# Optimization experiments

Measured on AMD Instinct MI355X. Metric: run time of the kernel, lower is better.

Reference implementation:

```python
import jax, jax.numpy as jnp
import numpy as np
import itertools

# ---- static configuration (matches init_kwargs) ----
LS = [0, 1, 2, 3]            # spherical harmonic degrees, parity (-1)^l
MUL = 128                    # channel multiplicity of hklm / output
N_EDGES = 16384
DIMS = [2 * l + 1 for l in LS]
Y_DIM = sum(DIMS)                        # 16
H_DIM = sum(d * MUL for d in DIMS)       # 2048
Y_OFF = np.cumsum([0] + DIMS).tolist()
H_OFF = np.cumsum([0] + [d * MUL for d in DIMS]).tolist()

# ---- real-basis O(3) Clebsch-Gordan coefficients (numpy, setup-time) ----
def _su2_generators(l):
    m = np.arange(-l, l + 1)
    Lz = np.diag(m).astype(np.complex128)
    vals = np.sqrt(l * (l + 1) - m[:-1] * (m[:-1] + 1))
    Lp = np.zeros((2 * l + 1, 2 * l + 1), np.complex128)
    Lp[np.arange(1, 2 * l + 1), np.arange(2 * l)] = vals
    Lm = Lp.T.copy()
    return (Lp + Lm) / 2.0, (Lp - Lm) / 2.0j, Lz

def _c2r(l):
    # unitary change of basis: complex SH -> real SH
    d = 2 * l + 1
    U = np.zeros((d, d), np.complex128)
    U[l, l] = 1.0
    s2 = 1.0 / np.sqrt(2.0)
    for m in range(1, l + 1):
        U[l + m, l + m] = (-1) ** m * s2
        U[l + m, l - m] = s2
        U[l - m, l + m] = -1j * (-1) ** m * s2
        U[l - m, l - m] = 1j * s2
    return U

def _real_generators(l):
    U = _c2r(l)
    return [np.real(-1j * (U @ L @ U.conj().T)) for L in _su2_generators(l)]

def _cg(l1, l2, l3):
    # invariant tensor = null space of the summed infinitesimal rotation action
    G1, G2, G3 = _real_generators(l1), _real_generators(l2), _real_generators(l3)
    d1, d2, d3 = 2 * l1 + 1, 2 * l2 + 1, 2 * l3 + 1
    I1, I2, I3 = np.eye(d1), np.eye(d2), np.eye(d3)
    rows = []
    for k in range(3):
        rows.append(np.kron(np.kron(G1[k], I2), I3)
                    + np.kron(np.kron(I1, G2[k]), I3)
                    + np.kron(np.kron(I1, I2), G3[k]))
    K = np.concatenate(rows, axis=0)
    _, s, Vt = np.linalg.svd(K)
    c = Vt[-1].reshape(d1, d2, d3)
    c = c / np.linalg.norm(c)
    c = c * np.sign(c.reshape(-1)[np.argmax(np.abs(c))])  # deterministic sign
    return c

PATHS = []
_CG_LIST = []
for (i1, l1), (i2, l2), (i3, l3) in itertools.product(enumerate(LS), enumerate(LS), enumerate(LS)):
    # triangle inequality + O3 parity selection rule ((-1)^l parities)
    if abs(l1 - l2) <= l3 <= l1 + l2 and (l1 + l2 + l3) % 2 == 0:
        PATHS.append((i1, i2, i3))
        _CG_LIST.append(_cg(l1, l2, l3))
N_PATHS = len(PATHS)                    # 23
W_DIM = N_PATHS * MUL                   # 2944
CG_OFF = np.cumsum([0] + [c.size for c in _CG_LIST]).tolist()
CGC_NP = np.concatenate([c.reshape(-1) for c in _CG_LIST]).astype(np.float32)


def setup_inputs() -> dict:
    key = jax.random.key(0)
    k1, k2, k3 = jax.random.split(key, 3)
    return {
        "Ylm": jax.random.normal(k1, (N_EDGES, Y_DIM), jnp.float32),
        "hklm": jax.random.normal(k2, (N_EDGES, H_DIM), jnp.float32),
        "weight": jax.random.normal(k3, (N_EDGES, W_DIM), jnp.float32),
        "CGC": jnp.asarray(CGC_NP),   # registered buffer in the torch module
    }


def reference(Ylm, hklm, weight, CGC):
    # segmented tensor product 'abcu,a,bu,cu' with per-path weight fused in:
    # out[n, c, u] += sum_{a,b} CG_p[a,b,c] * w_p[n,u] * Y[n,a] * h[n,b,u]
    N = Ylm.shape[0]
    out = jnp.zeros((N, H_DIM), Ylm.dtype)
    for p, (i1, i2, i3) in enumerate(PATHS):
        d1, d2, d3 = DIMS[i1], DIMS[i2], DIMS[i3]
        cg = CGC[CG_OFF[p]:CG_OFF[p + 1]].reshape(d1, d2, d3)
        y = Ylm[:, Y_OFF[i1]:Y_OFF[i1] + d1]
        h = hklm[:, H_OFF[i2]:H_OFF[i2] + d2 * MUL].reshape(N, d2, MUL)
        w = weight[:, p * MUL:(p + 1) * MUL]
        z = jnp.einsum('abc,na,nbu->ncu', cg, y, h) * w[:, None, :]
        out = out.at[:, H_OFF[i3]:H_OFF[i3] + d3 * MUL].add(z.reshape(N, d3 * MUL))
    return out
```

## Files before the change

### kernel.cpp

```cpp
#include <hip/hip_runtime.h>


#define BS 256
#define GSZ 32
#define EPB 8
#define YD 16
#define HD 2048
#define WD 2944
#define NP 23
#define NROW 99

typedef float f4 __attribute__((ext_vector_type(4)));

#define FOR_PATHS(X) \
  X(0, 0,0,0,    0,  0) \
  X(1, 0,1,1,    1,  1) \
  X(2, 0,2,2,   10,  4) \
  X(3, 0,3,3,   35,  9) \
  X(4, 1,0,1,   84, 16) \
  X(5, 1,1,0,   93, 19) \
  X(6, 1,1,2,  102, 20) \
  X(7, 1,2,1,  147, 25) \
  X(8, 1,2,3,  192, 28) \
  X(9, 1,3,2,  297, 35) \
  X(10,2,0,2,  402, 40) \
  X(11,2,1,1,  427, 45) \
  X(12,2,1,3,  472, 48) \
  X(13,2,2,0,  577, 55) \
  X(14,2,2,2,  602, 56) \
  X(15,2,3,1,  727, 61) \
  X(16,2,3,3,  832, 64) \
  X(17,3,0,3, 1077, 71) \
  X(18,3,1,2, 1126, 78) \
  X(19,3,2,1, 1231, 83) \
  X(20,3,2,3, 1336, 86) \
  X(21,3,3,0, 1581, 93) \
  X(22,3,3,2, 1630, 94)

__host__ __device__ constexpr int coff(int l) {
  return l == 0 ? 0 : (l == 1 ? 1 : (l == 2 ? 4 : 9));
}

__global__ __launch_bounds__(BS)
__attribute__((amdgpu_waves_per_eu(2, 2)))
void etp_kernel(
    const float* __restrict__ Y, const float* __restrict__ H,
    const float* __restrict__ W, const float* __restrict__ CG,
    float* __restrict__ O) {
  const int g = threadIdx.x >> 5;
  const int l = threadIdx.x & 31;
  const int n = blockIdx.x * EPB + g;

  __shared__ __align__(16) float Bsm[EPB][NROW * 8];
  __shared__ float ysm[EPB][YD];

  { const int t = threadIdx.x;
    if (t < EPB * YD) {
      const int e = t >> 4, c = t & 15;
      ysm[e][c] = Y[(size_t)(blockIdx.x * EPB + e) * YD + c];
    } }
  __syncthreads();

#define BUILD(P, L1, L2, L3, CGO, RO) { \
    constexpr int d1 = 2*(L1)+1, d2 = 2*(L2)+1, d3 = 2*(L3)+1; \
    _Pragma("unroll") \
    for (int it = 0; it < (d2 * d3 + GSZ - 1) / GSZ; ++it) { \
      const int idx = l + it * GSZ; \
      if (idx < d2 * d3) { \
        const int m3 = idx / d2, m2 = idx - m3 * d2; \
        float s = 0.f; \
        _Pragma("unroll") \
        for (int a = 0; a < d1; ++a) \
          s += CG[(CGO) + (a * d2 + m2) * d3 + m3] * ysm[g][coff(L1) + a]; \
        Bsm[g][((RO) + m3) * 8 + m2] = s; \
      } } }
  FOR_PATHS(BUILD)
#undef BUILD
  __syncthreads();

  const f4* __restrict__ Hp = (const f4*)(H + (size_t)n * HD);
  const f4* __restrict__ Wp = (const f4*)(W + (size_t)n * WD);
  f4* __restrict__ Op = (f4*)(O + (size_t)n * HD);

  f4 h[YD];
#pragma unroll
  for (int c = 0; c < YD; ++c) h[c] = Hp[c * GSZ + l];
  f4 wv[NP];
#pragma unroll
  for (int p = 0; p < NP; ++p) wv[p] = Wp[p * GSZ + l];

  f4 acc[YD];
#pragma unroll
  for (int c = 0; c < YD; ++c) acc[c] = (f4)0.f;

#define DOPATH(P, L1, L2, L3, CGO, RO) { \
    constexpr int d2 = 2*(L2)+1, d3 = 2*(L3)+1; \
    _Pragma("unroll") \
    for (int m3 = 0; m3 < d3; ++m3) { \
      const f4* row = (const f4*)&Bsm[g][((RO) + m3) * 8]; \
      float br[8]; \
      *(f4*)&br[0] = row[0]; \
      if (d2 > 4) *(f4*)&br[4] = row[1]; \
      f4 s = (f4)0.f; \
      _Pragma("unroll") \
      for (int m2 = 0; m2 < d2; ++m2) \
        s += br[m2] * h[coff(L2) + m2]; \
      acc[coff(L3) + m3] += s * wv[P]; \
    } }
  FOR_PATHS(DOPATH)
#undef DOPATH

#pragma unroll
  for (int c = 0; c < YD; ++c)
    __builtin_nontemporal_store(acc[c], &Op[c * GSZ + l]);
}

extern "C" void kernel_launch(void* const* d_in, const int* in_sizes, int n_in,
                              void* d_out, int out_size, void* d_ws, size_t ws_size,
                              hipStream_t stream) {
  const float* Y  = (const float*)d_in[0];
  const float* H  = (const float*)d_in[1];
  const float* W  = (const float*)d_in[2];
  const float* CG = (const float*)d_in[3];
  float* O = (float*)d_out;

  const int n_edges = in_sizes[0] / YD;
  etp_kernel<<<n_edges / EPB, BS, 0, stream>>>(Y, H, W, CG, O);
}
```

Baseline: 107.5 us.

## Map one thread per channel, two edges per block, group paths by input degree

Switches from 32 threads per edge holding four channels each as float4 to 128 threads per edge with one scalar channel each, and two edges per block instead of eight. Paths are regrouped by input degree so only that degree's h values stay live, and weights are loaded per path just before use. This cuts register pressure and raises occupancy (launch bounds allow 8 blocks) to hide memory latency better. In exchange it loses 128-bit vector loads and stores, and CG/Y basis building is spread over fewer edges per block.

```diff
diff --git a/kernel.cpp b/kernel.cpp
--- a/kernel.cpp
+++ b/kernel.cpp
@@ -2,12 +2,11 @@
 
 
 #define BS 256
-#define GSZ 32
-#define EPB 8
+#define EPB 2
+#define TPE 128
 #define YD 16
 #define HD 2048
 #define WD 2944
-#define NP 23
 #define NROW 99
 
 typedef float f4 __attribute__((ext_vector_type(4)));
@@ -41,15 +40,13 @@
   return l == 0 ? 0 : (l == 1 ? 1 : (l == 2 ? 4 : 9));
 }
 
-__global__ __launch_bounds__(BS)
-__attribute__((amdgpu_waves_per_eu(2, 2)))
-void etp_kernel(
+__global__ __launch_bounds__(BS, 8) void etp_kernel(
     const float* __restrict__ Y, const float* __restrict__ H,
     const float* __restrict__ W, const float* __restrict__ CG,
     float* __restrict__ O) {
-  const int g = threadIdx.x >> 5;
-  const int l = threadIdx.x & 31;
-  const int n = blockIdx.x * EPB + g;
+  const int g = threadIdx.x >> 7;
+  const int u = threadIdx.x & 127;
+  const size_t n = (size_t)blockIdx.x * EPB + g;
 
   __shared__ __align__(16) float Bsm[EPB][NROW * 8];
   __shared__ float ysm[EPB][YD];
@@ -63,56 +60,72 @@
 
 #define BUILD(P, L1, L2, L3, CGO, RO) { \
     constexpr int d1 = 2*(L1)+1, d2 = 2*(L2)+1, d3 = 2*(L3)+1; \
-    _Pragma("unroll") \
-    for (int it = 0; it < (d2 * d3 + GSZ - 1) / GSZ; ++it) { \
-      const int idx = l + it * GSZ; \
-      if (idx < d2 * d3) { \
-        const int m3 = idx / d2, m2 = idx - m3 * d2; \
-        float s = 0.f; \
-        _Pragma("unroll") \
-        for (int a = 0; a < d1; ++a) \
-          s += CG[(CGO) + (a * d2 + m2) * d3 + m3] * ysm[g][coff(L1) + a]; \
-        Bsm[g][((RO) + m3) * 8 + m2] = s; \
-      } } }
+    if (u < d2 * d3) { \
+      const int m3 = u / d2, m2 = u - m3 * d2; \
+      float s = 0.f; \
+      _Pragma("unroll") \
+      for (int a = 0; a < d1; ++a) \
+        s += CG[(CGO) + (a * d2 + m2) * d3 + m3] * ysm[g][coff(L1) + a]; \
+      Bsm[g][((RO) + m3) * 8 + m2] = s; \
+    } }
   FOR_PATHS(BUILD)
 #undef BUILD
   __syncthreads();
 
-  const f4* __restrict__ Hp = (const f4*)(H + (size_t)n * HD);
-  const f4* __restrict__ Wp = (const f4*)(W + (size_t)n * WD);
-  f4* __restrict__ Op = (f4*)(O + (size_t)n * HD);
+  const float* __restrict__ Hn = H + n * HD + u;
+  const float* __restrict__ Wn = W + n * WD + u;
+  float* __restrict__ On = O + n * HD + u;
 
-  f4 h[YD];
+  float acc[YD];
 #pragma unroll
-  for (int c = 0; c < YD; ++c) h[c] = Hp[c * GSZ + l];
-  f4 wv[NP];
-#pragma unroll
-  for (int p = 0; p < NP; ++p) wv[p] = Wp[p * GSZ + l];
+  for (int c = 0; c < YD; ++c) acc[c] = 0.f;
 
-  f4 acc[YD];
-#pragma unroll
-  for (int c = 0; c < YD; ++c) acc[c] = (f4)0.f;
-
-#define DOPATH(P, L1, L2, L3, CGO, RO) { \
+#define DOP(P, L2, L3, RO) { \
     constexpr int d2 = 2*(L2)+1, d3 = 2*(L3)+1; \
+    const float wv = Wn[(P) * TPE]; \
     _Pragma("unroll") \
     for (int m3 = 0; m3 < d3; ++m3) { \
       const f4* row = (const f4*)&Bsm[g][((RO) + m3) * 8]; \
       float br[8]; \
       *(f4*)&br[0] = row[0]; \
       if (d2 > 4) *(f4*)&br[4] = row[1]; \
-      f4 s = (f4)0.f; \
+      float s = 0.f; \
       _Pragma("unroll") \
-      for (int m2 = 0; m2 < d2; ++m2) \
-        s += br[m2] * h[coff(L2) + m2]; \
-      acc[coff(L3) + m3] += s * wv[P]; \
+      for (int m2 = 0; m2 < d2; ++m2) s += br[m2] * hh[m2]; \
+      acc[coff(L3) + m3] += s * wv; \
     } }
-  FOR_PATHS(DOPATH)
-#undef DOPATH
+
+  {
+    float hh[1];
+    hh[0] = Hn[(coff(0) + 0) * TPE];
+    DOP(0, 0, 0, 0)  DOP(4, 0, 1, 16)  DOP(10, 0, 2, 40)  DOP(17, 0, 3, 71)
+  }
+  {
+    float hh[3];
+#pragma unroll
+    for (int m = 0; m < 3; ++m) hh[m] = Hn[(coff(1) + m) * TPE];
+    DOP(1, 1, 1, 1)  DOP(5, 1, 0, 19)  DOP(6, 1, 2, 20)
+    DOP(11, 1, 1, 45)  DOP(12, 1, 3, 48)  DOP(18, 1, 2, 78)
+  }
+  {
+    float hh[5];
+#pragma unroll
+    for (int m = 0; m < 5; ++m) hh[m] = Hn[(coff(2) + m) * TPE];
+    DOP(2, 2, 2, 4)  DOP(7, 2, 1, 25)  DOP(8, 2, 3, 28)
+    DOP(13, 2, 0, 55)  DOP(14, 2, 2, 56)  DOP(19, 2, 1, 83)  DOP(20, 2, 3, 86)
+  }
+  {
+    float hh[7];
+#pragma unroll
+    for (int m = 0; m < 7; ++m) hh[m] = Hn[(coff(3) + m) * TPE];
+    DOP(3, 3, 3, 9)  DOP(9, 3, 2, 35)  DOP(15, 3, 1, 61)
+    DOP(16, 3, 3, 64)  DOP(21, 3, 0, 93)  DOP(22, 3, 2, 94)
+  }
+#undef DOP
 
 #pragma unroll
   for (int c = 0; c < YD; ++c)
-    __builtin_nontemporal_store(acc[c], &Op[c * GSZ + l]);
+    __builtin_nontemporal_store(acc[c], &On[c * TPE]);
 }
 
 extern "C" void kernel_launch(void* const* d_in, const int* in_sizes, int n_in,
```

After: 101.9 us. -5.2%, faster.
